# Kernel tuning notes

Hardware: AMD Instinct MI355X
Metric: run time of the kernel (lower is better)

The kernel has to match this reference:

```python
import jax, jax.numpy as jnp
import numpy as np

N_HEADS = 4
D_K = 32

def setup_inputs() -> dict:
    key = jax.random.key(0)
    k1, k2, k3 = jax.random.split(key, 3)
    B, C, H, W = 4, 128, 64, 64
    x = jax.random.normal(k1, (B, C, H, W), dtype=jnp.float32)
    # projection: Linear(C, n_heads*d_k*3)
    Wp = jax.random.normal(k2, (N_HEADS * D_K * 3, C), dtype=jnp.float32) * (1.0 / np.sqrt(C))
    bp = jnp.zeros((N_HEADS * D_K * 3,), dtype=jnp.float32)
    # output: Linear(n_heads*d_k, C)
    Wo = jax.random.normal(k3, (C, N_HEADS * D_K), dtype=jnp.float32) * (1.0 / np.sqrt(N_HEADS * D_K))
    bo = jnp.zeros((C,), dtype=jnp.float32)
    return {"x": x, "Wp": Wp, "bp": bp, "Wo": Wo, "bo": bo}

def reference(x, Wp, bp, Wo, bo):
    B, C, H, W = x.shape
    scale = D_K ** (-0.5)
    # (B, C, H, W) -> (B, N, C);  NOTE: self.norm is defined but never applied in the original forward
    xs = x.reshape(B, C, H * W).transpose(0, 2, 1)
    qkv = (xs @ Wp.T + bp).reshape(B, H * W, N_HEADS, 3 * D_K)
    q, k, v = jnp.split(qkv, 3, axis=-1)  # each (B, N, h, d)
    attn = jnp.einsum('bihd,bjhd->bijh', q, k) * scale
    # faithful to original: softmax over dim=1 (the query/i axis)
    attn = jax.nn.softmax(attn, axis=1)
    res = jnp.einsum('bijh,bjhd->bihd', attn, v).reshape(B, H * W, N_HEADS * D_K)
    res = res @ Wo.T + bo + xs
    return res.transpose(0, 2, 1).reshape(B, C, H, W)
```

## Files before the change

kernel.cpp:

```cpp
#include <hip/hip_runtime.h>

typedef __bf16 bf16_t;
typedef __bf16 bf16x8 __attribute__((ext_vector_type(8)));
typedef float  f32x4  __attribute__((ext_vector_type(4)));
typedef unsigned u32x4 __attribute__((ext_vector_type(4)));

#define MFMA16(a, b, c) __builtin_amdgcn_mfma_f32_16x16x32_bf16((a), (b), (c), 0, 0, 0)

__device__ __forceinline__ float exp2_f(float x) { return __builtin_amdgcn_exp2f(x); }

union BPack { bf16_t h[2]; unsigned u; };

constexpr int Bn = 4, Cc = 128, Nn = 4096, NH = 4, DK = 32;
constexpr float QSCALE = 0.176776695f * 1.44269504f;

__global__ __launch_bounds__(256) void k_qkv(const float* __restrict__ x,
                                             const float* __restrict__ Wp,
                                             const float* __restrict__ bp,
                                             bf16_t* __restrict__ q_s,
                                             bf16_t* __restrict__ k_s,
                                             bf16_t* __restrict__ vt_s)
{
    __shared__ __attribute__((aligned(16))) char smem[40960];
    const int n0 = blockIdx.x * 64;
    const int b  = blockIdx.y;
    const int h  = blockIdx.z;
    const int t  = threadIdx.x;
    const int w = t >> 6, lane = t & 63, a = lane & 15, g = lane >> 4;

    const float* xb = x + (size_t)b * Cc * Nn;
    #pragma unroll
    for (int it = 0; it < 16; ++it) {
        int c = ((t >> 6) + it * 4) * 2;
        int n = t & 63;
        BPack p;
        p.h[0] = (bf16_t)xb[(size_t)c * Nn + n0 + n];
        p.h[1] = (bf16_t)xb[(size_t)(c + 1) * Nn + n0 + n];
        unsigned byte = n * 256 + ((unsigned)(c * 2) ^ ((n & 7) << 4));
        *(unsigned*)(smem + byte) = p.u;
    }
    const float* wpg = Wp + (size_t)h * 96 * Cc;
    #pragma unroll
    for (int it = 0; it < 24; ++it) {
        int idx = t + it * 256;
        int row = idx >> 6;
        int col = (idx & 63) * 2;
        BPack p;
        p.h[0] = (bf16_t)wpg[row * Cc + col];
        p.h[1] = (bf16_t)wpg[row * Cc + col + 1];
        unsigned byte = 16384 + row * 256 + ((unsigned)(col * 2) ^ ((row & 7) << 4));
        *(unsigned*)(smem + byte) = p.u;
    }
    __syncthreads();

    f32x4 acc[6] = {};
    #pragma unroll
    for (int kc = 0; kc < 4; ++kc) {
        int cb = (kc * 32 + g * 8) * 2;
        int rowA = w * 16 + a;
        bf16x8 af = *(const bf16x8*)(smem + rowA * 256 + (cb ^ ((rowA & 7) << 4)));
        #pragma unroll
        for (int pt = 0; pt < 6; ++pt) {
            int rowB = pt * 16 + a;
            bf16x8 bfr = *(const bf16x8*)(smem + 16384 + rowB * 256 + (cb ^ ((rowB & 7) << 4)));
            acc[pt] = MFMA16(af, bfr, acc[pt]);
        }
    }

    const int bh = b * NH + h;
    #pragma unroll
    for (int pt = 0; pt < 4; ++pt) {
        const int which = pt >> 1;
        const int d = (pt & 1) * 16 + a;
        const float bias = bp[h * 96 + which * 32 + d];
        bf16_t* dst = which ? k_s : q_s;
        const float sc = which ? 1.0f : QSCALE;
        #pragma unroll
        for (int r = 0; r < 4; ++r) {
            int n = n0 + w * 16 + g * 4 + r;
            dst[((size_t)bh * Nn + n) * DK + d] = (bf16_t)((acc[pt][r] + bias) * sc);
        }
    }
    __syncthreads();
    bf16_t* vt_l = (bf16_t*)smem;
    #pragma unroll
    for (int pt = 4; pt < 6; ++pt) {
        const int d = (pt & 1) * 16 + a;
        const float bias = bp[h * 96 + 64 + d];
        #pragma unroll
        for (int r = 0; r < 4; ++r) {
            int nl = w * 16 + g * 4 + r;
            vt_l[d * 72 + nl] = (bf16_t)(acc[pt][r] + bias);
        }
    }
    __syncthreads();
    #pragma unroll
    for (int it = 0; it < 8; ++it) {
        int idx = t + it * 256;
        int d = idx >> 6, n = idx & 63;
        int m = n & 31;
        int col = ((m & 15) << 1) | (m >> 4);
        int jj = (n & 32) | col;
        vt_s[((size_t)bh * DK + d) * Nn + n0 + jj] = vt_l[d * 72 + n];
    }
}

__global__ __launch_bounds__(256) void k_stats(const bf16_t* __restrict__ q_s,
                                               const bf16_t* __restrict__ k_s,
                                               float* __restrict__ S_part)
{
    const int bx = blockIdx.x;
    const int is = bx & 3;
    const int jc = (bx >> 2) & 31;
    const int bh = bx >> 7;
    const int t = threadIdx.x, w = t >> 6, lane = t & 63, a = lane & 15, g = lane >> 4;
    const bf16_t* Q = q_s + (size_t)bh * Nn * DK;
    const bf16_t* K = k_s + (size_t)bh * Nn * DK;
    const int jb = jc * 128 + w * 32;
    bf16x8 kf0 = *(const bf16x8*)(K + (jb + a) * DK + g * 8);
    bf16x8 kf1 = *(const bf16x8*)(K + (jb + 16 + a) * DK + g * 8);
    f32x4 l0 = {}, l1 = {}, l2 = {}, l3 = {};
    const int ilo = is * (Nn / 4);
    #pragma unroll 2
    for (int i0 = ilo; i0 < ilo + Nn / 4; i0 += 32) {
        bf16x8 qfA = *(const bf16x8*)(Q + (i0 + a) * DK + g * 8);
        bf16x8 qfB = *(const bf16x8*)(Q + (i0 + 16 + a) * DK + g * 8);
        f32x4 z = {};
        f32x4 t0 = MFMA16(qfA, kf0, z);
        f32x4 t1 = MFMA16(qfA, kf1, z);
        f32x4 t2 = MFMA16(qfB, kf0, z);
        f32x4 t3 = MFMA16(qfB, kf1, z);
        #pragma unroll
        for (int r = 0; r < 4; ++r) {
            l0[r] += exp2_f(t0[r]);
            l1[r] += exp2_f(t1[r]);
            l2[r] += exp2_f(t2[r]);
            l3[r] += exp2_f(t3[r]);
        }
    }
    l0 += l2;
    l1 += l3;
    float s0 = l0[0] + l0[1] + l0[2] + l0[3];
    float s1 = l1[0] + l1[1] + l1[2] + l1[3];
    s0 += __shfl_xor(s0, 16);
    s0 += __shfl_xor(s0, 32);
    s1 += __shfl_xor(s1, 16);
    s1 += __shfl_xor(s1, 32);
    if (g == 0) {
        float* Sp = S_part + ((size_t)is * 16 + bh) * Nn;
        Sp[jb + a]      = s0;
        Sp[jb + 16 + a] = s1;
    }
}

__global__ __launch_bounds__(256) void k_vscale(const float* __restrict__ S_part,
                                                bf16_t* __restrict__ vt_s)
{
    __shared__ float sinv[512];
    const int Jb = blockIdx.x;
    const int bh = blockIdx.y;
    const int t = threadIdx.x;
    if (t < 128) {
        #pragma unroll
        for (int k2 = 0; k2 < 4; ++k2) {
            int Jl = t * 4 + k2;
            int m = Jl & 31;
            int pJ = (Jl & ~31) | (m >> 1) | ((m & 1) << 4);
            int J = Jb * 512 + pJ;
            float s = 0.f;
            #pragma unroll
            for (int is = 0; is < 4; ++is)
                s += S_part[((size_t)is * 16 + bh) * Nn + J];
            sinv[Jl] = 1.0f / s;
        }
    }
    __syncthreads();
    bf16_t* vrow = vt_s + (size_t)bh * DK * Nn;
    #pragma unroll
    for (int it = 0; it < 8; ++it) {
        int idx = t + it * 256;
        int d = idx >> 6, Jg = (idx & 63) * 8;
        bf16_t* p = vrow + (size_t)d * Nn + Jb * 512 + Jg;
        bf16x8 v = *(const bf16x8*)p;
        #pragma unroll
        for (int k2 = 0; k2 < 8; ++k2) v[k2] = (bf16_t)((float)v[k2] * sinv[Jg + k2]);
        *(bf16x8*)p = v;
    }
}

template<int JSPAN>
__global__ __launch_bounds__(256, 4) void k_attn(const bf16_t* __restrict__ q_s,
                                                 const bf16_t* __restrict__ k_s,
                                                 const bf16_t* __restrict__ vt_s,
                                                 unsigned* __restrict__ opart)
{
    constexpr int NJS = Nn / JSPAN;
    const int bx = blockIdx.x;
    const int js = bx % NJS;
    const int ic = (bx / NJS) & 15;
    const int bh = bx / (NJS * 16);
    const int b = bh >> 2, h = bh & 3;
    const int t = threadIdx.x, w = t >> 6, lane = t & 63, a = lane & 15, g = lane >> 4;
    const int ib = ic * 256 + w * 64;
    const bf16_t* Q  = q_s  + (size_t)bh * Nn * DK;
    const bf16_t* K  = k_s  + (size_t)bh * Nn * DK;
    const bf16_t* Vt = vt_s + (size_t)bh * DK * Nn;
    bf16x8 qf[4];
    #pragma unroll
    for (int it = 0; it < 4; ++it)
        qf[it] = *(const bf16x8*)(Q + (size_t)(ib + it * 16 + a) * DK + g * 8);
    f32x4 o0[4] = {}, o1[4] = {};
    auto compute = [&](bf16x8 ck0, bf16x8 ck1, bf16x8 cv0, bf16x8 cv1) {
        f32x4 z = {};
        __builtin_amdgcn_s_setprio(1);
        #pragma unroll
        for (int it = 0; it < 4; ++it) {
            f32x4 s0 = MFMA16(ck0, qf[it], z);
            f32x4 s1 = MFMA16(ck1, qf[it], z);
            bf16x8 pa;
            #pragma unroll
            for (int r = 0; r < 4; ++r) {
                pa[2 * r]     = (bf16_t)exp2_f(s0[r]);
                pa[2 * r + 1] = (bf16_t)exp2_f(s1[r]);
            }
            o0[it] = MFMA16(pa, cv0, o0[it]);
            o1[it] = MFMA16(pa, cv1, o1[it]);
        }
        __builtin_amdgcn_s_setprio(0);
    };
    const int jlo = js * JSPAN;
    bf16x8 kf0 = *(const bf16x8*)(K + (size_t)(jlo + a) * DK + g * 8);
    bf16x8 kf1 = *(const bf16x8*)(K + (size_t)(jlo + 16 + a) * DK + g * 8);
    bf16x8 vf0 = *(const bf16x8*)(Vt + (size_t)a * Nn + jlo + g * 8);
    bf16x8 vf1 = *(const bf16x8*)(Vt + (size_t)(16 + a) * Nn + jlo + g * 8);
    #pragma unroll 2
    for (int j0 = jlo; j0 < jlo + JSPAN - 32; j0 += 32) {
        bf16x8 ck0 = kf0, ck1 = kf1, cv0 = vf0, cv1 = vf1;
        kf0 = *(const bf16x8*)(K + (size_t)(j0 + 32 + a) * DK + g * 8);
        kf1 = *(const bf16x8*)(K + (size_t)(j0 + 48 + a) * DK + g * 8);
        vf0 = *(const bf16x8*)(Vt + (size_t)a * Nn + j0 + 32 + g * 8);
        vf1 = *(const bf16x8*)(Vt + (size_t)(16 + a) * Nn + j0 + 32 + g * 8);
        compute(ck0, ck1, cv0, cv1);
    }
    compute(kf0, kf1, vf0, vf1);

    unsigned* Ob = opart + ((size_t)(js * Bn + b) * Nn) * 64 + h * 16 + a;
    #pragma unroll
    for (int it = 0; it < 4; ++it) {
        #pragma unroll
        for (int r = 0; r < 4; ++r) {
            int n = ib + it * 16 + g * 4 + r;
            BPack p;
            p.h[0] = (bf16_t)o0[it][r];
            p.h[1] = (bf16_t)o1[it][r];
            Ob[(size_t)n * 64] = p.u;
        }
    }
}

template<int NJS>
__global__ __launch_bounds__(256) void k_out(const unsigned* __restrict__ opart,
                                             const float* __restrict__ Wo,
                                             const float* __restrict__ bo,
                                             const float* __restrict__ x,
                                             float* __restrict__ out)
{
    __shared__ __attribute__((aligned(16))) char smem[33280];
    const int n0 = blockIdx.x * 64;
    const int b = blockIdx.y;
    const int t = threadIdx.x, w = t >> 6, lane = t & 63, a = lane & 15, g = lane >> 4;
    #pragma unroll
    for (int it = 0; it < 32; ++it) {
        int idx = t + it * 256;
        int row = idx >> 6;
        int col = (idx & 63) * 2;
        BPack p;
        p.h[0] = (bf16_t)Wo[row * 128 + col];
        p.h[1] = (bf16_t)Wo[row * 128 + col + 1];
        unsigned byte = row * 256 + ((unsigned)(col * 2) ^ ((row & 7) << 4));
        *(unsigned*)(smem + byte) = p.u;
    }
    __syncthreads();
    const size_t OSTR32 = (size_t)Bn * Nn * 64;
    const unsigned* Ob = opart + ((size_t)b * Nn + n0 + w * 16 + a) * 64;
    const unsigned hi = (g >= 2);
    const int wsub = (g & 1) * 8;
    f32x4 acc[8] = {};
    #pragma unroll
    for (int kc = 0; kc < 4; ++kc) {
        float s[8] = {};
        #pragma unroll
        for (int js = 0; js < NJS; ++js) {
            const unsigned* pp = Ob + (size_t)js * OSTR32 + kc * 16 + wsub;
            u32x4 v0 = *(const u32x4*)pp;
            u32x4 v1 = *(const u32x4*)(pp + 4);
            #pragma unroll
            for (int k2 = 0; k2 < 4; ++k2) {
                s[k2]     += __uint_as_float(hi ? (v0[k2] & 0xffff0000u) : (v0[k2] << 16));
                s[k2 + 4] += __uint_as_float(hi ? (v1[k2] & 0xffff0000u) : (v1[k2] << 16));
            }
        }
        bf16x8 af;
        #pragma unroll
        for (int k2 = 0; k2 < 8; ++k2) af[k2] = (bf16_t)s[k2];
        int cb = (kc * 32 + g * 8) * 2;
        #pragma unroll
        for (int ct = 0; ct < 8; ++ct) {
            int rowB = ct * 16 + a;
            bf16x8 bfr = *(const bf16x8*)(smem + rowB * 256 + (cb ^ ((rowB & 7) << 4)));
            acc[ct] = MFMA16(af, bfr, acc[ct]);
        }
    }
    __syncthreads();
    float* out_t = (float*)smem;
    #pragma unroll
    for (int ct = 0; ct < 8; ++ct) {
        int c = ct * 16 + a;
        #pragma unroll
        for (int r = 0; r < 4; ++r) {
            out_t[c * 65 + w * 16 + g * 4 + r] = acc[ct][r];
        }
    }
    __syncthreads();
    const float* xb = x + (size_t)b * Cc * Nn;
    #pragma unroll
    for (int it = 0; it < 32; ++it) {
        int idx = t + it * 256;
        int c = idx >> 6, n = idx & 63;
        out[((size_t)b * Cc + c) * Nn + n0 + n] = out_t[c * 65 + n] + xb[(size_t)c * Nn + n0 + n] + bo[c];
    }
}

extern "C" void kernel_launch(void* const* d_in, const int* in_sizes, int n_in,
                              void* d_out, int out_size, void* d_ws, size_t ws_size,
                              hipStream_t stream)
{
    const float* x  = (const float*)d_in[0];
    const float* Wp = (const float*)d_in[1];
    const float* bp = (const float*)d_in[2];
    const float* Wo = (const float*)d_in[3];
    const float* bo = (const float*)d_in[4];
    float* out = (float*)d_out;

    char* ws = (char*)d_ws;
    bf16_t*  q_s   = (bf16_t*)(ws);
    bf16_t*  k_s   = (bf16_t*)(ws + (4  << 20));
    bf16_t*  vt_s  = (bf16_t*)(ws + (8  << 20));
    float*   S_part= (float*) (ws + (12 << 20));
    unsigned* opart= (unsigned*)(ws + (13 << 20));

    const size_t base = 13ull << 20;
    const size_t plane = 4ull << 20;
    int NJS = 1;
    if (ws_size >= base + 4 * plane) NJS = 4;
    else if (ws_size >= base + 2 * plane) NJS = 2;

    k_qkv   <<<dim3(Nn / 64, Bn, NH),   256, 0, stream>>>(x, Wp, bp, q_s, k_s, vt_s);
    k_stats <<<16 * 32 * 4,             256, 0, stream>>>(q_s, k_s, S_part);
    k_vscale<<<dim3(8, 16),             256, 0, stream>>>(S_part, vt_s);
    if (NJS == 4) {
        k_attn<1024><<<16 * 16 * 4, 256, 0, stream>>>(q_s, k_s, vt_s, opart);
        k_out<4><<<dim3(Nn / 64, Bn), 256, 0, stream>>>(opart, Wo, bo, x, out);
    } else if (NJS == 2) {
        k_attn<2048><<<16 * 16 * 2, 256, 0, stream>>>(q_s, k_s, vt_s, opart);
        k_out<2><<<dim3(Nn / 64, Bn), 256, 0, stream>>>(opart, Wo, bo, x, out);
    } else {
        k_attn<4096><<<16 * 16 * 1, 256, 0, stream>>>(q_s, k_s, vt_s, opart);
        k_out<1><<<dim3(Nn / 64, Bn), 256, 0, stream>>>(opart, Wo, bo, x, out);
    }
}
```

Measured before the change: 191.1 us.

## Swizzle block order across XCDs and double-buffer K/V prefetch in attention

Remaps blockIdx in k_stats and k_attn so that consecutive logical blocks land on the same XCD (bid&7 interleave), which should improve L2 reuse of Q/K/V per head. In k_attn, the K/V register prefetch goes from one stage to two stages (64 columns ahead), so global load latency is better hidden, at the cost of more VGPRs. The s_setprio boosts around the MFMA compute are also removed. Higher register pressure could cut occupancy under launch_bounds(256,4).

```diff
diff --git a/kernel.cpp b/kernel.cpp
--- a/kernel.cpp
+++ b/kernel.cpp
@@ -109,7 +109,8 @@
                                                const bf16_t* __restrict__ k_s,
                                                float* __restrict__ S_part)
 {
-    const int bx = blockIdx.x;
+    const int bid = blockIdx.x;
+    const int bx = (bid & 7) * 256 + (bid >> 3);
     const int is = bx & 3;
     const int jc = (bx >> 2) & 31;
     const int bh = bx >> 7;
@@ -195,7 +196,9 @@
                                                  unsigned* __restrict__ opart)
 {
     constexpr int NJS = Nn / JSPAN;
-    const int bx = blockIdx.x;
+    constexpr int NWG = 16 * 16 * NJS;
+    const int bid = blockIdx.x;
+    const int bx = (bid & 7) * (NWG / 8) + (bid >> 3);
     const int js = bx % NJS;
     const int ic = (bx / NJS) & 15;
     const int bh = bx / (NJS * 16);
@@ -212,7 +215,6 @@
     f32x4 o0[4] = {}, o1[4] = {};
     auto compute = [&](bf16x8 ck0, bf16x8 ck1, bf16x8 cv0, bf16x8 cv1) {
         f32x4 z = {};
-        __builtin_amdgcn_s_setprio(1);
         #pragma unroll
         for (int it = 0; it < 4; ++it) {
             f32x4 s0 = MFMA16(ck0, qf[it], z);
@@ -226,23 +228,29 @@
             o0[it] = MFMA16(pa, cv0, o0[it]);
             o1[it] = MFMA16(pa, cv1, o1[it]);
         }
-        __builtin_amdgcn_s_setprio(0);
     };
     const int jlo = js * JSPAN;
-    bf16x8 kf0 = *(const bf16x8*)(K + (size_t)(jlo + a) * DK + g * 8);
-    bf16x8 kf1 = *(const bf16x8*)(K + (size_t)(jlo + 16 + a) * DK + g * 8);
-    bf16x8 vf0 = *(const bf16x8*)(Vt + (size_t)a * Nn + jlo + g * 8);
-    bf16x8 vf1 = *(const bf16x8*)(Vt + (size_t)(16 + a) * Nn + jlo + g * 8);
-    #pragma unroll 2
-    for (int j0 = jlo; j0 < jlo + JSPAN - 32; j0 += 32) {
-        bf16x8 ck0 = kf0, ck1 = kf1, cv0 = vf0, cv1 = vf1;
-        kf0 = *(const bf16x8*)(K + (size_t)(j0 + 32 + a) * DK + g * 8);
-        kf1 = *(const bf16x8*)(K + (size_t)(j0 + 48 + a) * DK + g * 8);
-        vf0 = *(const bf16x8*)(Vt + (size_t)a * Nn + j0 + 32 + g * 8);
-        vf1 = *(const bf16x8*)(Vt + (size_t)(16 + a) * Nn + j0 + 32 + g * 8);
-        compute(ck0, ck1, cv0, cv1);
-    }
-    compute(kf0, kf1, vf0, vf1);
+    #define LOADJ(K0, K1, V0, V1, J) \
+        K0 = *(const bf16x8*)(K + (size_t)((J) + a) * DK + g * 8); \
+        K1 = *(const bf16x8*)(K + (size_t)((J) + 16 + a) * DK + g * 8); \
+        V0 = *(const bf16x8*)(Vt + (size_t)a * Nn + (J) + g * 8); \
+        V1 = *(const bf16x8*)(Vt + (size_t)(16 + a) * Nn + (J) + g * 8)
+
+    bf16x8 kA0, kA1, vA0, vA1, kB0, kB1, vB0, vB1;
+    LOADJ(kA0, kA1, vA0, vA1, jlo);
+    LOADJ(kB0, kB1, vB0, vB1, jlo + 32);
+    #pragma unroll 1
+    for (int j0 = jlo; j0 < jlo + JSPAN - 64; j0 += 64) {
+        bf16x8 t0 = kA0, t1 = kA1, t2 = vA0, t3 = vA1;
+        LOADJ(kA0, kA1, vA0, vA1, j0 + 64);
+        compute(t0, t1, t2, t3);
+        bf16x8 u0 = kB0, u1 = kB1, u2 = vB0, u3 = vB1;
+        LOADJ(kB0, kB1, vB0, vB1, j0 + 96);
+        compute(u0, u1, u2, u3);
+    }
+    compute(kA0, kA1, vA0, vA1);
+    compute(kB0, kB1, vB0, vB1);
+    #undef LOADJ
 
     unsigned* Ob = opart + ((size_t)(js * Bn + b) * Nn) * 64 + h * 16 + a;
     #pragma unroll
```

Result: no change. 190.8 us (-0.2%).
